# Optimization experiments

Measured on AMD Instinct MI355X. Metric: run time of the kernel, lower is better.

Reference implementation:

```python
import jax, jax.numpy as jnp
import numpy as np

HIDDEN = 256
HEADS = 8
HEAD_DIM = HIDDEN // HEADS
SCALE = HEAD_DIM ** -0.5


def setup_inputs() -> dict:
    key = jax.random.key(0)
    ks = jax.random.split(key, 12)
    B, N = 2, 2048
    s = lambda fan_in: 1.0 / np.sqrt(fan_in)
    inp = {
        'x': jax.random.normal(ks[0], (B, N, HIDDEN), jnp.float32),
        'coords': jax.random.normal(ks[1], (B, N, 3), jnp.float32),
        'W_qkv': jax.random.normal(ks[2], (HIDDEN, 3 * HIDDEN), jnp.float32) * s(HIDDEN),
        'W_out': jax.random.normal(ks[3], (HIDDEN, HIDDEN), jnp.float32) * s(HIDDEN),
        'b_out': jnp.zeros((HIDDEN,), jnp.float32),
        'pos_w1': jax.random.normal(ks[4], (3, 16), jnp.float32) * s(3),
        'pos_b1': jnp.zeros((16,), jnp.float32),
        'pos_w2': jax.random.normal(ks[5], (16, HEADS), jnp.float32) * s(16),
        'pos_b2': jnp.zeros((HEADS,), jnp.float32),
        'sym_w1': jax.random.normal(ks[6], (3, 16), jnp.float32) * s(3),
        'sym_b1': jnp.zeros((16,), jnp.float32),
        'sym_w2': jax.random.normal(ks[7], (16, HEADS), jnp.float32) * s(16),
        'sym_b2': jnp.zeros((HEADS,), jnp.float32),
    }
    return inp


def _bias_mlp(rel, w1, b1, w2, b2):
    # rel: [B,N,N,3] -> [B,H,N,N]
    h = jax.nn.relu(jnp.einsum('bijc,ck->bijk', rel, w1) + b1)
    out = jnp.einsum('bijk,kh->bijh', h, w2) + b2
    return jnp.transpose(out, (0, 3, 1, 2))


def reference(x, coords, W_qkv, W_out, b_out, pos_w1, pos_b1, pos_w2, pos_b2,
              sym_w1, sym_b1, sym_w2, sym_b2):
    B, N, C = x.shape
    qkv = (x @ W_qkv).reshape(B, N, 3, HEADS, HEAD_DIM)
    qkv = jnp.transpose(qkv, (2, 0, 3, 1, 4))  # [3,B,H,N,D]
    q, k, v = qkv[0], qkv[1], qkv[2]
    dots = jnp.einsum('bhid,bhjd->bhij', q, k) * SCALE
    rel_pos = coords[:, :, None, :] - coords[:, None, :, :]  # [B,N,N,3]
    reflect = jnp.array([-1.0, 1.0, 1.0], dtype=coords.dtype)
    coords_sym = coords * reflect
    sym_rel_pos = coords[:, :, None, :] - coords_sym[:, None, :, :]
    bias_direct = _bias_mlp(rel_pos, pos_w1, pos_b1, pos_w2, pos_b2)
    bias_sym = _bias_mlp(sym_rel_pos, sym_w1, sym_b1, sym_w2, sym_b2)
    attn = jax.nn.softmax(dots + bias_direct + bias_sym, axis=-1)
    out = jnp.einsum('bhij,bhjd->bhid', attn, v)
    out = jnp.transpose(out, (0, 2, 1, 3)).reshape(B, N, C)
    return out @ W_out + b_out
```

## Files before the change

kernel.cpp:

```cpp
#include <hip/hip_runtime.h>
#include <hip/hip_fp16.h>

typedef _Float16 half8_t __attribute__((ext_vector_type(8)));
typedef _Float16 half4_t __attribute__((ext_vector_type(4)));
typedef _Float16 h2      __attribute__((ext_vector_type(2)));
typedef float    f32x4   __attribute__((ext_vector_type(4)));

#define LOG2E 1.4426950408889634f
#define KSCALE (0.17677669529663687f * LOG2E)

#if __has_builtin(__builtin_amdgcn_exp2f)
#define EXP2F(x) __builtin_amdgcn_exp2f(x)
#else
#define EXP2F(x) exp2f(x)
#endif

template <int N>
__device__ __forceinline__ int dpp_ror(int v) {
  return __builtin_amdgcn_update_dpp(0, v, 0x120 + N, 0xf, 0xf, true);
}
__device__ __forceinline__ h2 rowmax16_h2(h2 v) {
  int t;
  t = dpp_ror<1>(__builtin_bit_cast(int, v));
  v = __builtin_elementwise_max(v, __builtin_bit_cast(h2, t));
  t = dpp_ror<2>(__builtin_bit_cast(int, v));
  v = __builtin_elementwise_max(v, __builtin_bit_cast(h2, t));
  t = dpp_ror<4>(__builtin_bit_cast(int, v));
  v = __builtin_elementwise_max(v, __builtin_bit_cast(h2, t));
  t = dpp_ror<8>(__builtin_bit_cast(int, v));
  v = __builtin_elementwise_max(v, __builtin_bit_cast(h2, t));
  return v;
}

__global__ __launch_bounds__(256) void prep_misc(
    const float* __restrict__ Wqkv, const float* __restrict__ Wout,
    const float* __restrict__ coords,
    const float* __restrict__ pw1, const float* __restrict__ pb1,
    const float* __restrict__ sw1, const float* __restrict__ sb1,
    _Float16* __restrict__ WqkvT, _Float16* __restrict__ WoutT,
    _Float16* __restrict__ APre, _Float16* __restrict__ BPre)
{
  __shared__ float tile[64][65];
  const int bi = blockIdx.x, tid = threadIdx.x;
  if (bi < 64) {
    const float* src; _Float16* dst; int t, W;
    if (bi < 48) { t = bi;      src = Wqkv; dst = WqkvT; W = 768; }
    else         { t = bi - 48; src = Wout; dst = WoutT; W = 256; }
    const int nOT = W >> 6;
    const int tk = t / nOT, to = t % nOT;
    const int cx = tid & 63, ry = tid >> 6;
#pragma unroll
    for (int rr = 0; rr < 16; ++rr) {
      const int kl = rr * 4 + ry;
      tile[kl][cx] = src[(tk * 64 + kl) * W + to * 64 + cx];
    }
    __syncthreads();
#pragma unroll
    for (int rr = 0; rr < 16; ++rr) {
      const int ol = rr * 4 + ry;
      dst[(to * 64 + ol) * 256 + tk * 64 + cx] = (_Float16)tile[cx][ol];
    }
  } else {
    const int row = (bi - 64) * 256 + tid;
    const float c0 = coords[row * 3 + 0];
    const float c1 = coords[row * 3 + 1];
    const float c2 = coords[row * 3 + 2];
#pragma unroll
    for (int k = 0; k < 16; ++k) {
      float a = c0 * pw1[k] + c1 * pw1[16 + k] + c2 * pw1[32 + k];
      APre[row * 32 + k] = (_Float16)(a + pb1[k]);
      BPre[row * 32 + k] = (_Float16)a;
      float s  =  c0 * sw1[k] + c1 * sw1[16 + k] + c2 * sw1[32 + k];
      float sb = -c0 * sw1[k] + c1 * sw1[16 + k] + c2 * sw1[32 + k];
      APre[row * 32 + 16 + k] = (_Float16)(s + sb1[k]);
      BPre[row * 32 + 16 + k] = (_Float16)sb;
    }
  }
}

__global__ __launch_bounds__(256) void qkv_gemm(
    const float* __restrict__ x, const _Float16* __restrict__ WqkvT,
    _Float16* __restrict__ Qh, _Float16* __restrict__ Kh,
    _Float16* __restrict__ Vt)
{
  __shared__ __align__(16) _Float16 tbuf[4][1536];
  const int wv = threadIdx.x >> 6;
  const int wg = blockIdx.x * 4 + wv;
  const int ti = wg / 12, og = wg % 12;
  const int i0 = ti * 16, o0 = og * 64;
  const int lane = threadIdx.x & 63, q = lane >> 4, c = lane & 15;
  f32x4 acc[4] = {{0,0,0,0},{0,0,0,0},{0,0,0,0},{0,0,0,0}};
  const float*    arow = x + (i0 + c) * 256;
  const _Float16* brow = WqkvT + (o0 + c) * 256;
#pragma unroll
  for (int k0 = 0; k0 < 256; k0 += 32) {
    f32x4 a0 = *reinterpret_cast<const f32x4*>(arow + k0 + q * 8);
    f32x4 a1 = *reinterpret_cast<const f32x4*>(arow + k0 + q * 8 + 4);
    half8_t af;
    af[0] = (_Float16)a0[0]; af[1] = (_Float16)a0[1];
    af[2] = (_Float16)a0[2]; af[3] = (_Float16)a0[3];
    af[4] = (_Float16)a1[0]; af[5] = (_Float16)a1[1];
    af[6] = (_Float16)a1[2]; af[7] = (_Float16)a1[3];
#pragma unroll
    for (int t = 0; t < 4; ++t) {
      half8_t bf = *reinterpret_cast<const half8_t*>(brow + t * 16 * 256 + k0 + q * 8);
      acc[t] = __builtin_amdgcn_mfma_f32_16x16x32_f16(af, bf, acc[t], 0, 0, 0);
    }
  }
  const int b = i0 >> 11, n0 = i0 & 2047;
  _Float16* vt = tbuf[wv];
  if (og < 8) {
#pragma unroll
    for (int t = 0; t < 4; ++t)
#pragma unroll
      for (int r = 0; r < 4; ++r)
        vt[(q * 4 + r) * 72 + t * 16 + c] = (_Float16)acc[t][r];
    asm volatile("s_waitcnt lgkmcnt(0)" ::: "memory");
    __builtin_amdgcn_sched_barrier(0);
    const int nl = lane & 15, seg = lane >> 4;
    const int o_g = o0 + seg * 16;
    const int h = (o_g >> 5) & 7, dbase = o_g & 31;
    _Float16* dst = ((o_g >> 8) == 0 ? Qh : Kh) +
                    ((b * 8 + h) * 2048 + n0 + nl) * 32 + dbase;
    half8_t r0 = *reinterpret_cast<const half8_t*>(vt + nl * 72 + seg * 16);
    half8_t r1 = *reinterpret_cast<const half8_t*>(vt + nl * 72 + seg * 16 + 8);
    *reinterpret_cast<half8_t*>(dst)     = r0;
    *reinterpret_cast<half8_t*>(dst + 8) = r1;
  } else {
#pragma unroll
    for (int t = 0; t < 4; ++t)
#pragma unroll
      for (int r = 0; r < 4; ++r)
        vt[(t * 16 + c) * 24 + q * 4 + r] = (_Float16)acc[t][r];
    asm volatile("s_waitcnt lgkmcnt(0)" ::: "memory");
    __builtin_amdgcn_sched_barrier(0);
    const long row = (long)(b * 256 + (o0 - 512) + lane);
    half8_t r0 = *reinterpret_cast<const half8_t*>(vt + lane * 24);
    half8_t r1 = *reinterpret_cast<const half8_t*>(vt + lane * 24 + 8);
    *reinterpret_cast<half8_t*>(Vt + row * 2048 + n0)     = r0;
    *reinterpret_cast<half8_t*>(Vt + row * 2048 + n0 + 8) = r1;
  }
}

__global__ __launch_bounds__(512, 4) void flash(
    const _Float16* __restrict__ Qh, const _Float16* __restrict__ Kh,
    const _Float16* __restrict__ Vt, const _Float16* __restrict__ APre,
    const _Float16* __restrict__ BPre, const float* __restrict__ pw2,
    const float* __restrict__ sw2, _Float16* __restrict__ Opart,
    float* __restrict__ Mpart)
{
  __shared__ __align__(16) unsigned char smem[53504];
  _Float16* biasH = reinterpret_cast<_Float16*>(smem);
  _Float16* pbuf  = reinterpret_cast<_Float16*>(smem + 37120);

  const int blk = blockIdx.x;
  const int b     = blk >> 8;
  const int chunk = (blk >> 6) & 3;
  const int i0    = (blk & 63) << 5;
  const int tid = threadIdx.x;
  const int w = tid >> 6, lane = tid & 63;
  const int q = lane >> 4, c = lane & 15;

  const _Float16* qbase = Qh + ((b * 8 + w) * 2048 + i0) * 32;
  half8_t qfA = *reinterpret_cast<const half8_t*>(qbase + c * 32 + q * 8);
  half8_t qfB = *reinterpret_cast<const half8_t*>(qbase + (16 + c) * 32 + q * 8);
  const _Float16* abase = APre + (b * 2048 + i0) * 32;
  half8_t apfA = *reinterpret_cast<const half8_t*>(abase + c * 32 + q * 8);
  half8_t apfB = *reinterpret_cast<const half8_t*>(abase + (16 + c) * 32 + q * 8);

  half8_t w2f;
#pragma unroll
  for (int jj = 0; jj < 8; ++jj) {
    const int k = q * 8 + jj;
    float val = 0.f;
    if (c < 8) val = (k < 16 ? pw2[k * 8 + c] : sw2[(k - 16) * 8 + c]) * LOG2E;
    w2f[jj] = (_Float16)val;
  }
  half8_t ones8;
#pragma unroll
  for (int jj = 0; jj < 8; ++jj) ones8[jj] = (_Float16)1.0f;

  float mA[4], mB[4];
  f32x4 O0A = {0,0,0,0}, O1A = {0,0,0,0}, O0B = {0,0,0,0}, O1B = {0,0,0,0};
  f32x4 lpA = {0,0,0,0}, lpB = {0,0,0,0};
#pragma unroll
  for (int r = 0; r < 4; ++r) { mA[r] = 0.f; mB[r] = 0.f; }

  const f32x4 z4 = {0.f, 0.f, 0.f, 0.f};
  half8_t hzero8 = {};

  const int jbase = chunk * 512;
  const _Float16* BPre_b = BPre + (long)b * 2048 * 32;

  const int bwoff = c * 1160 + w * 144 + q * 4;
  const int broff = w * 1160 + c * 72 + q * 4;
  _Float16* pbA = pbuf + w * 1024;
  _Float16* pbB = pbA + 512;
  const int pwo = q * 128 + 2 * c;
  const int pro = c * 32 + q * 8;
  const _Float16* kb0 = Kh + ((b * 8 + w) * 2048 + jbase) * 32;
  const _Float16* vb0 = Vt + (b * 8 + w) * 65536 + jbase;
  const int ko0 = (2 * c) * 32 + q * 8, ko1 = ko0 + 32;
  const int vo0 = c * 2048 + q * 8,     vo1 = vo0 + 16 * 2048;
  const _Float16* bpb = BPre_b + (jbase + w * 4) * 32 + q * 8;

  auto bias_prod = [&](_Float16* bH, half8_t f0, half8_t f1, half8_t f2,
                       half8_t f3) {
    _Float16* bW = bH + bwoff;
#pragma unroll
    for (int mt = 0; mt < 4; ++mt) {
      half8_t bpf = (mt == 0) ? f0 : (mt == 1) ? f1 : (mt == 2) ? f2 : f3;
      half8_t hvA = __builtin_elementwise_max(apfA - bpf, hzero8);
      f32x4 bcA = __builtin_amdgcn_mfma_f32_16x16x32_f16(hvA, w2f, z4, 0, 0, 0);
      half8_t hvB = __builtin_elementwise_max(apfB - bpf, hzero8);
      f32x4 bcB = __builtin_amdgcn_mfma_f32_16x16x32_f16(hvB, w2f, z4, 0, 0, 0);
      if (c < 8) {
        half4_t b4;
        b4[0] = (_Float16)bcA[0]; b4[1] = (_Float16)bcA[1];
        b4[2] = (_Float16)bcA[2]; b4[3] = (_Float16)bcA[3];
        *reinterpret_cast<half4_t*>(bW + mt * 36) = b4;
        half4_t b5;
        b5[0] = (_Float16)bcB[0]; b5[1] = (_Float16)bcB[1];
        b5[2] = (_Float16)bcB[2]; b5[3] = (_Float16)bcB[3];
        *reinterpret_cast<half4_t*>(bW + mt * 36 + 16) = b5;
      }
    }
  };

  {
    half8_t t0 = *reinterpret_cast<const half8_t*>(bpb);
    half8_t t1 = *reinterpret_cast<const half8_t*>(bpb + 32);
    half8_t t2 = *reinterpret_cast<const half8_t*>(bpb + 64);
    half8_t t3 = *reinterpret_cast<const half8_t*>(bpb + 96);
    bias_prod(biasH, t0, t1, t2, t3);
  }
  half8_t pf0 = *reinterpret_cast<const half8_t*>(bpb + 1024);
  half8_t pf1 = *reinterpret_cast<const half8_t*>(bpb + 1024 + 32);
  half8_t pf2 = *reinterpret_cast<const half8_t*>(bpb + 1024 + 64);
  half8_t pf3 = *reinterpret_cast<const half8_t*>(bpb + 1024 + 96);
  __syncthreads();

  auto tile = [&](const int jt, _Float16* bufR, _Float16* bufW,
                  const bool last) {
    const _Float16* bR = bufR + broff;
    half4_t bbA0 = *reinterpret_cast<const half4_t*>(bR);
    half4_t bbA1 = *reinterpret_cast<const half4_t*>(bR + 36);
    half4_t bbB0 = *reinterpret_cast<const half4_t*>(bR + 16);
    half4_t bbB1 = *reinterpret_cast<const half4_t*>(bR + 52);

    if (!last) bias_prod(bufW, pf0, pf1, pf2, pf3);

    {
      const int jn = (jt + 2 < 16) ? (jt + 2) : 15;
      const _Float16* bp = bpb + jn * 1024;
      pf0 = *reinterpret_cast<const half8_t*>(bp);
      pf1 = *reinterpret_cast<const half8_t*>(bp + 32);
      pf2 = *reinterpret_cast<const half8_t*>(bp + 64);
      pf3 = *reinterpret_cast<const half8_t*>(bp + 96);
    }

    const _Float16* kbase = kb0 + jt * 1024;
    const _Float16* vbase = vb0 + jt * 32;
    half8_t kf0 = *reinterpret_cast<const half8_t*>(kbase + ko0);
    half8_t kf1 = *reinterpret_cast<const half8_t*>(kbase + ko1);
    half8_t vf0 = *reinterpret_cast<const half8_t*>(vbase + vo0);
    half8_t vf1 = *reinterpret_cast<const half8_t*>(vbase + vo1);
    f32x4 sA0 = __builtin_amdgcn_mfma_f32_16x16x32_f16(qfA, kf0, z4, 0, 0, 0);
    f32x4 sA1 = __builtin_amdgcn_mfma_f32_16x16x32_f16(qfA, kf1, z4, 0, 0, 0);
    f32x4 sB0 = __builtin_amdgcn_mfma_f32_16x16x32_f16(qfB, kf0, z4, 0, 0, 0);
    f32x4 sB1 = __builtin_amdgcn_mfma_f32_16x16x32_f16(qfB, kf1, z4, 0, 0, 0);

    {
      float svm0[4], svm1[4], p0[4], p1[4];
#pragma unroll
      for (int r = 0; r < 4; ++r) {
        const float bm0 = (float)bbA0[r] - mA[r];
        const float bm1 = (float)bbA1[r] - mA[r];
        svm0[r] = fmaf(sA0[r], KSCALE, bm0);
        svm1[r] = fmaf(sA1[r], KSCALE, bm1);
        p0[r] = EXP2F(svm0[r]);
        p1[r] = EXP2F(svm1[r]);
      }
      float need = fmaxf(fmaxf(fmaxf(svm0[0], svm1[0]), fmaxf(svm0[1], svm1[1])),
                         fmaxf(fmaxf(svm0[2], svm1[2]), fmaxf(svm0[3], svm1[3])));
      if (__any(need > 4.0f)) {
        float mr[4];
#pragma unroll
        for (int r = 0; r < 4; ++r) mr[r] = fmaxf(svm0[r], svm1[r]) + mA[r];
        h2 pk01, pk23;
        pk01[0] = (_Float16)mr[0]; pk01[1] = (_Float16)mr[1];
        pk23[0] = (_Float16)mr[2]; pk23[1] = (_Float16)mr[3];
        pk01 = rowmax16_h2(pk01);
        pk23 = rowmax16_h2(pk23);
        float mred[4] = {(float)pk01[0], (float)pk01[1],
                         (float)pk23[0], (float)pk23[1]};
#pragma unroll
        for (int r = 0; r < 4; ++r) {
          const float mnew = fmaxf(mA[r], mred[r]);
          const float alpha = EXP2F(mA[r] - mnew);
          p0[r] *= alpha; p1[r] *= alpha;
          lpA[r] *= alpha;
          O0A[r] *= alpha; O1A[r] *= alpha;
          mA[r] = mnew;
        }
      }
#pragma unroll
      for (int r = 0; r < 4; ++r) {
        h2 pp; pp[0] = (_Float16)p0[r]; pp[1] = (_Float16)p1[r];
        *reinterpret_cast<h2*>(pbA + pwo + r * 32) = pp;
      }
    }
    {
      float svm0[4], svm1[4], p0[4], p1[4];
#pragma unroll
      for (int r = 0; r < 4; ++r) {
        const float bm0 = (float)bbB0[r] - mB[r];
        const float bm1 = (float)bbB1[r] - mB[r];
        svm0[r] = fmaf(sB0[r], KSCALE, bm0);
        svm1[r] = fmaf(sB1[r], KSCALE, bm1);
        p0[r] = EXP2F(svm0[r]);
        p1[r] = EXP2F(svm1[r]);
      }
      float need = fmaxf(fmaxf(fmaxf(svm0[0], svm1[0]), fmaxf(svm0[1], svm1[1])),
                         fmaxf(fmaxf(svm0[2], svm1[2]), fmaxf(svm0[3], svm1[3])));
      if (__any(need > 4.0f)) {
        float mr[4];
#pragma unroll
        for (int r = 0; r < 4; ++r) mr[r] = fmaxf(svm0[r], svm1[r]) + mB[r];
        h2 pk01, pk23;
        pk01[0] = (_Float16)mr[0]; pk01[1] = (_Float16)mr[1];
        pk23[0] = (_Float16)mr[2]; pk23[1] = (_Float16)mr[3];
        pk01 = rowmax16_h2(pk01);
        pk23 = rowmax16_h2(pk23);
        float mred[4] = {(float)pk01[0], (float)pk01[1],
                         (float)pk23[0], (float)pk23[1]};
#pragma unroll
        for (int r = 0; r < 4; ++r) {
          const float mnew = fmaxf(mB[r], mred[r]);
          const float alpha = EXP2F(mB[r] - mnew);
          p0[r] *= alpha; p1[r] *= alpha;
          lpB[r] *= alpha;
          O0B[r] *= alpha; O1B[r] *= alpha;
          mB[r] = mnew;
        }
      }
#pragma unroll
      for (int r = 0; r < 4; ++r) {
        h2 pp; pp[0] = (_Float16)p0[r]; pp[1] = (_Float16)p1[r];
        *reinterpret_cast<h2*>(pbB + pwo + r * 32) = pp;
      }
    }

    asm volatile("s_waitcnt lgkmcnt(0)" ::: "memory");
    __builtin_amdgcn_sched_barrier(0);

    half8_t pfAx = *reinterpret_cast<const half8_t*>(pbA + pro);
    half8_t pfBx = *reinterpret_cast<const half8_t*>(pbB + pro);
    O0A = __builtin_amdgcn_mfma_f32_16x16x32_f16(pfAx, vf0, O0A, 0, 0, 0);
    O1A = __builtin_amdgcn_mfma_f32_16x16x32_f16(pfAx, vf1, O1A, 0, 0, 0);
    O0B = __builtin_amdgcn_mfma_f32_16x16x32_f16(pfBx, vf0, O0B, 0, 0, 0);
    O1B = __builtin_amdgcn_mfma_f32_16x16x32_f16(pfBx, vf1, O1B, 0, 0, 0);
    lpA = __builtin_amdgcn_mfma_f32_16x16x32_f16(pfAx, ones8, lpA, 0, 0, 0);
    lpB = __builtin_amdgcn_mfma_f32_16x16x32_f16(pfBx, ones8, lpB, 0, 0, 0);

    if (!last) __syncthreads();
  };

  for (int pt = 0; pt < 8; ++pt) {
    tile(2 * pt,     biasH,        biasH + 9280, false);
    tile(2 * pt + 1, biasH + 9280, biasH,        pt == 7);
  }

#pragma unroll
  for (int r = 0; r < 4; ++r) {
    const float s = lpA[r];
    const float inv = 1.f / s;
    const int n = i0 + q * 4 + r;
    const long base = (long)(((chunk * 2 + b) * 8 + w) * 2048 + n);
    Opart[base * 32 + c]      = (_Float16)(O0A[r] * inv);
    Opart[base * 32 + 16 + c] = (_Float16)(O1A[r] * inv);
    if (c == 0) Mpart[base] = mA[r] + __log2f(s);
  }
#pragma unroll
  for (int r = 0; r < 4; ++r) {
    const float s = lpB[r];
    const float inv = 1.f / s;
    const int n = i0 + 16 + q * 4 + r;
    const long base = (long)(((chunk * 2 + b) * 8 + w) * 2048 + n);
    Opart[base * 32 + c]      = (_Float16)(O0B[r] * inv);
    Opart[base * 32 + 16 + c] = (_Float16)(O1B[r] * inv);
    if (c == 0) Mpart[base] = mB[r] + __log2f(s);
  }
}

__global__ __launch_bounds__(256) void combine_proj(
    const _Float16* __restrict__ Opart, const float* __restrict__ Mpart,
    const _Float16* __restrict__ WoutT, const float* __restrict__ bout,
    float* __restrict__ out)
{
  __shared__ _Float16 aT[16][264];
  const int i0 = blockIdx.x * 16;
  const int b = i0 >> 11;
  const int n0 = i0 & 2047;
  const int tid = threadIdx.x;
  {
    const int row = tid >> 4, cg = tid & 15;
    const int n = n0 + row;
    const int h = cg >> 1;
    const int d0 = (cg & 1) * 16;
    float mv[4], M = -INFINITY;
#pragma unroll
    for (int ck = 0; ck < 4; ++ck) {
      mv[ck] = Mpart[((ck * 2 + b) * 8 + h) * 2048 + n];
      M = fmaxf(M, mv[ck]);
    }
    float num[16];
#pragma unroll
    for (int e = 0; e < 16; ++e) num[e] = 0.f;
    float den = 0.f;
#pragma unroll
    for (int ck = 0; ck < 4; ++ck) {
      const float wgt = EXP2F(mv[ck] - M);
      const _Float16* op = Opart +
          (long)(((ck * 2 + b) * 8 + h) * 2048 + n) * 32 + d0;
      half8_t o0v = *reinterpret_cast<const half8_t*>(op);
      half8_t o1v = *reinterpret_cast<const half8_t*>(op + 8);
#pragma unroll
      for (int e = 0; e < 8; ++e) {
        num[e]     += wgt * (float)o0v[e];
        num[8 + e] += wgt * (float)o1v[e];
      }
      den += wgt;
    }
    const float inv = 1.f / den;
    half8_t h0, h1;
#pragma unroll
    for (int e = 0; e < 8; ++e) {
      h0[e] = (_Float16)(num[e] * inv);
      h1[e] = (_Float16)(num[8 + e] * inv);
    }
    *reinterpret_cast<half8_t*>(&aT[row][cg * 16])     = h0;
    *reinterpret_cast<half8_t*>(&aT[row][cg * 16 + 8]) = h1;
  }
  __syncthreads();

  const int o0 = (tid >> 6) * 64;
  const int lane = tid & 63, q = lane >> 4, c = lane & 15;
  f32x4 acc[4] = {{0,0,0,0},{0,0,0,0},{0,0,0,0},{0,0,0,0}};
  const _Float16* brow = WoutT + (o0 + c) * 256;
#pragma unroll
  for (int k0 = 0; k0 < 256; k0 += 32) {
    half8_t af = *reinterpret_cast<const half8_t*>(&aT[c][k0 + q * 8]);
#pragma unroll
    for (int t = 0; t < 4; ++t) {
      half8_t bf = *reinterpret_cast<const half8_t*>(brow + t * 16 * 256 + k0 + q * 8);
      acc[t] = __builtin_amdgcn_mfma_f32_16x16x32_f16(af, bf, acc[t], 0, 0, 0);
    }
  }
#pragma unroll
  for (int t = 0; t < 4; ++t) {
    const float bo = bout[o0 + t * 16 + c];
#pragma unroll
    for (int r = 0; r < 4; ++r)
      out[(i0 + q * 4 + r) * 256 + o0 + t * 16 + c] = acc[t][r] + bo;
  }
}

extern "C" void kernel_launch(void* const* d_in, const int* in_sizes, int n_in,
                              void* d_out, int out_size, void* d_ws, size_t ws_size,
                              hipStream_t stream)
{
  const float* x      = (const float*)d_in[0];
  const float* coords = (const float*)d_in[1];
  const float* Wqkv   = (const float*)d_in[2];
  const float* Wout   = (const float*)d_in[3];
  const float* bout   = (const float*)d_in[4];
  const float* pw1    = (const float*)d_in[5];
  const float* pb1    = (const float*)d_in[6];
  const float* pw2    = (const float*)d_in[7];
  const float* sw1    = (const float*)d_in[9];
  const float* sb1    = (const float*)d_in[10];
  const float* sw2    = (const float*)d_in[11];
  float* out = (float*)d_out;

  char* ws = (char*)d_ws;
  _Float16* Qh      = (_Float16*)(ws + 0);
  _Float16* Kh      = (_Float16*)(ws + 2097152);
  _Float16* Vt      = (_Float16*)(ws + 4194304);
  _Float16* WqkvT   = (_Float16*)(ws + 8388608);
  _Float16* WoutT   = (_Float16*)(ws + 8781824);
  _Float16* APre    = (_Float16*)(ws + 8912896);
  _Float16* BPre    = (_Float16*)(ws + 9175040);
  _Float16* Opart   = (_Float16*)(ws + 9437184);
  float*    Mpart   = (float*)   (ws + 17825792);

  prep_misc<<<80, 256, 0, stream>>>(Wqkv, Wout, coords, pw1, pb1, sw1, sb1,
                                    WqkvT, WoutT, APre, BPre);
  qkv_gemm<<<768, 256, 0, stream>>>(x, WqkvT, Qh, Kh, Vt);
  flash<<<512, 512, 0, stream>>>(Qh, Kh, Vt, APre, BPre, pw2, sw2, Opart, Mpart);
  combine_proj<<<256, 256, 0, stream>>>(Opart, Mpart, WoutT, bout, out);
}
```

Before: 163.6 us.

## Prefetch next K/V fragments and defer bias production until after PV MFMAs

Loads the K and V fragments for the next tile one iteration ahead, so the QK MFMAs no longer wait on global loads. The two A/B softmax halves are merged into one pass that shares a single wave-wide rescale check. The bias MLP production for the tile after next, plus its prefetch, moves after the PV MFMAs so it can overlap with them. This raises register pressure, and reordering the bias writes before the barrier could shift LDS contention.

Result: slower. 202.9 us (+24.0%).

```diff
diff --git a/kernel.cpp b/kernel.cpp
--- a/kernel.cpp
+++ b/kernel.cpp
@@ -227,6 +227,13 @@
     }
   };
 
+  half8_t kfP0, kfP1, vfP0, vfP1;
+  half8_t pf0, pf1, pf2, pf3;
+
+  kfP0 = *reinterpret_cast<const half8_t*>(kb0 + ko0);
+  kfP1 = *reinterpret_cast<const half8_t*>(kb0 + ko1);
+  vfP0 = *reinterpret_cast<const half8_t*>(vb0 + vo0);
+  vfP1 = *reinterpret_cast<const half8_t*>(vb0 + vo1);
   {
     half8_t t0 = *reinterpret_cast<const half8_t*>(bpb);
     half8_t t1 = *reinterpret_cast<const half8_t*>(bpb + 32);
@@ -234,10 +241,10 @@
     half8_t t3 = *reinterpret_cast<const half8_t*>(bpb + 96);
     bias_prod(biasH, t0, t1, t2, t3);
   }
-  half8_t pf0 = *reinterpret_cast<const half8_t*>(bpb + 1024);
-  half8_t pf1 = *reinterpret_cast<const half8_t*>(bpb + 1024 + 32);
-  half8_t pf2 = *reinterpret_cast<const half8_t*>(bpb + 1024 + 64);
-  half8_t pf3 = *reinterpret_cast<const half8_t*>(bpb + 1024 + 96);
+  pf0 = *reinterpret_cast<const half8_t*>(bpb + 1024);
+  pf1 = *reinterpret_cast<const half8_t*>(bpb + 1024 + 32);
+  pf2 = *reinterpret_cast<const half8_t*>(bpb + 1024 + 64);
+  pf3 = *reinterpret_cast<const half8_t*>(bpb + 1024 + 96);
   __syncthreads();
 
   auto tile = [&](const int jt, _Float16* bufR, _Float16* bufW,
@@ -248,107 +255,77 @@
     half4_t bbB0 = *reinterpret_cast<const half4_t*>(bR + 16);
     half4_t bbB1 = *reinterpret_cast<const half4_t*>(bR + 52);
 
-    if (!last) bias_prod(bufW, pf0, pf1, pf2, pf3);
-
-    {
-      const int jn = (jt + 2 < 16) ? (jt + 2) : 15;
-      const _Float16* bp = bpb + jn * 1024;
-      pf0 = *reinterpret_cast<const half8_t*>(bp);
-      pf1 = *reinterpret_cast<const half8_t*>(bp + 32);
-      pf2 = *reinterpret_cast<const half8_t*>(bp + 64);
-      pf3 = *reinterpret_cast<const half8_t*>(bp + 96);
-    }
-
-    const _Float16* kbase = kb0 + jt * 1024;
-    const _Float16* vbase = vb0 + jt * 32;
-    half8_t kf0 = *reinterpret_cast<const half8_t*>(kbase + ko0);
-    half8_t kf1 = *reinterpret_cast<const half8_t*>(kbase + ko1);
-    half8_t vf0 = *reinterpret_cast<const half8_t*>(vbase + vo0);
-    half8_t vf1 = *reinterpret_cast<const half8_t*>(vbase + vo1);
+    half8_t kf0 = kfP0, kf1 = kfP1, vf0 = vfP0, vf1 = vfP1;
     f32x4 sA0 = __builtin_amdgcn_mfma_f32_16x16x32_f16(qfA, kf0, z4, 0, 0, 0);
     f32x4 sA1 = __builtin_amdgcn_mfma_f32_16x16x32_f16(qfA, kf1, z4, 0, 0, 0);
     f32x4 sB0 = __builtin_amdgcn_mfma_f32_16x16x32_f16(qfB, kf0, z4, 0, 0, 0);
     f32x4 sB1 = __builtin_amdgcn_mfma_f32_16x16x32_f16(qfB, kf1, z4, 0, 0, 0);
 
     {
-      float svm0[4], svm1[4], p0[4], p1[4];
-#pragma unroll
-      for (int r = 0; r < 4; ++r) {
-        const float bm0 = (float)bbA0[r] - mA[r];
-        const float bm1 = (float)bbA1[r] - mA[r];
-        svm0[r] = fmaf(sA0[r], KSCALE, bm0);
-        svm1[r] = fmaf(sA1[r], KSCALE, bm1);
-        p0[r] = EXP2F(svm0[r]);
-        p1[r] = EXP2F(svm1[r]);
-      }
-      float need = fmaxf(fmaxf(fmaxf(svm0[0], svm1[0]), fmaxf(svm0[1], svm1[1])),
-                         fmaxf(fmaxf(svm0[2], svm1[2]), fmaxf(svm0[3], svm1[3])));
-      if (__any(need > 4.0f)) {
-        float mr[4];
-#pragma unroll
-        for (int r = 0; r < 4; ++r) mr[r] = fmaxf(svm0[r], svm1[r]) + mA[r];
-        h2 pk01, pk23;
-        pk01[0] = (_Float16)mr[0]; pk01[1] = (_Float16)mr[1];
-        pk23[0] = (_Float16)mr[2]; pk23[1] = (_Float16)mr[3];
-        pk01 = rowmax16_h2(pk01);
-        pk23 = rowmax16_h2(pk23);
-        float mred[4] = {(float)pk01[0], (float)pk01[1],
-                         (float)pk23[0], (float)pk23[1]};
+      const int jn = last ? jt : jt + 1;
+      const _Float16* kbase = kb0 + jn * 1024;
+      const _Float16* vbase = vb0 + jn * 32;
+      kfP0 = *reinterpret_cast<const half8_t*>(kbase + ko0);
+      kfP1 = *reinterpret_cast<const half8_t*>(kbase + ko1);
+      vfP0 = *reinterpret_cast<const half8_t*>(vbase + vo0);
+      vfP1 = *reinterpret_cast<const half8_t*>(vbase + vo1);
+    }
+
+    float pA0[4], pA1[4], pB0[4], pB1[4];
+    float svA0[4], svA1[4], svB0[4], svB1[4];
+#pragma unroll
+    for (int r = 0; r < 4; ++r) {
+      svA0[r] = fmaf(sA0[r], KSCALE, (float)bbA0[r] - mA[r]);
+      svA1[r] = fmaf(sA1[r], KSCALE, (float)bbA1[r] - mA[r]);
+      svB0[r] = fmaf(sB0[r], KSCALE, (float)bbB0[r] - mB[r]);
+      svB1[r] = fmaf(sB1[r], KSCALE, (float)bbB1[r] - mB[r]);
+      pA0[r] = EXP2F(svA0[r]);
+      pA1[r] = EXP2F(svA1[r]);
+      pB0[r] = EXP2F(svB0[r]);
+      pB1[r] = EXP2F(svB1[r]);
+    }
+    {
+      float needA = fmaxf(fmaxf(fmaxf(svA0[0], svA1[0]), fmaxf(svA0[1], svA1[1])),
+                          fmaxf(fmaxf(svA0[2], svA1[2]), fmaxf(svA0[3], svA1[3])));
+      float needB = fmaxf(fmaxf(fmaxf(svB0[0], svB1[0]), fmaxf(svB0[1], svB1[1])),
+                          fmaxf(fmaxf(svB0[2], svB1[2]), fmaxf(svB0[3], svB1[3])));
+      if (__any(fmaxf(needA, needB) > 4.0f)) {
+        float mrA[4], mrB[4];
 #pragma unroll
         for (int r = 0; r < 4; ++r) {
-          const float mnew = fmaxf(mA[r], mred[r]);
-          const float alpha = EXP2F(mA[r] - mnew);
-          p0[r] *= alpha; p1[r] *= alpha;
-          lpA[r] *= alpha;
-          O0A[r] *= alpha; O1A[r] *= alpha;
-          mA[r] = mnew;
+          mrA[r] = fmaxf(svA0[r], svA1[r]) + mA[r];
+          mrB[r] = fmaxf(svB0[r], svB1[r]) + mB[r];
+        }
+        h2 a01, a23, b01, b23;
+        a01[0] = (_Float16)mrA[0]; a01[1] = (_Float16)mrA[1];
+        a23[0] = (_Float16)mrA[2]; a23[1] = (_Float16)mrA[3];
+        b01[0] = (_Float16)mrB[0]; b01[1] = (_Float16)mrB[1];
+        b23[0] = (_Float16)mrB[2]; b23[1] = (_Float16)mrB[3];
+        a01 = rowmax16_h2(a01); a23 = rowmax16_h2(a23);
+        b01 = rowmax16_h2(b01); b23 = rowmax16_h2(b23);
+        float mredA[4] = {(float)a01[0], (float)a01[1], (float)a23[0], (float)a23[1]};
+        float mredB[4] = {(float)b01[0], (float)b01[1], (float)b23[0], (float)b23[1]};
+#pragma unroll
+        for (int r = 0; r < 4; ++r) {
+          const float mnA = fmaxf(mA[r], mredA[r]);
+          const float aA = EXP2F(mA[r] - mnA);
+          pA0[r] *= aA; pA1[r] *= aA;
+          lpA[r] *= aA; O0A[r] *= aA; O1A[r] *= aA;
+          mA[r] = mnA;
+          const float mnB = fmaxf(mB[r], mredB[r]);
+          const float aB = EXP2F(mB[r] - mnB);
+          pB0[r] *= aB; pB1[r] *= aB;
+          lpB[r] *= aB; O0B[r] *= aB; O1B[r] *= aB;
+          mB[r] = mnB;
         }
       }
-#pragma unroll
-      for (int r = 0; r < 4; ++r) {
-        h2 pp; pp[0] = (_Float16)p0[r]; pp[1] = (_Float16)p1[r];
-        *reinterpret_cast<h2*>(pbA + pwo + r * 32) = pp;
-      }
-    }
-    {
-      float svm0[4], svm1[4], p0[4], p1[4];
-#pragma unroll
-      for (int r = 0; r < 4; ++r) {
-        const float bm0 = (float)bbB0[r] - mB[r];
-        const float bm1 = (float)bbB1[r] - mB[r];
-        svm0[r] = fmaf(sB0[r], KSCALE, bm0);
-        svm1[r] = fmaf(sB1[r], KSCALE, bm1);
-        p0[r] = EXP2F(svm0[r]);
-        p1[r] = EXP2F(svm1[r]);
-      }
-      float need = fmaxf(fmaxf(fmaxf(svm0[0], svm1[0]), fmaxf(svm0[1], svm1[1])),
-                         fmaxf(fmaxf(svm0[2], svm1[2]), fmaxf(svm0[3], svm1[3])));
-      if (__any(need > 4.0f)) {
-        float mr[4];
-#pragma unroll
-        for (int r = 0; r < 4; ++r) mr[r] = fmaxf(svm0[r], svm1[r]) + mB[r];
-        h2 pk01, pk23;
-        pk01[0] = (_Float16)mr[0]; pk01[1] = (_Float16)mr[1];
-        pk23[0] = (_Float16)mr[2]; pk23[1] = (_Float16)mr[3];
-        pk01 = rowmax16_h2(pk01);
-        pk23 = rowmax16_h2(pk23);
-        float mred[4] = {(float)pk01[0], (float)pk01[1],
-                         (float)pk23[0], (float)pk23[1]};
-#pragma unroll
-        for (int r = 0; r < 4; ++r) {
-          const float mnew = fmaxf(mB[r], mred[r]);
-          const float alpha = EXP2F(mB[r] - mnew);
-          p0[r] *= alpha; p1[r] *= alpha;
-          lpB[r] *= alpha;
-          O0B[r] *= alpha; O1B[r] *= alpha;
-          mB[r] = mnew;
-        }
-      }
-#pragma unroll
-      for (int r = 0; r < 4; ++r) {
-        h2 pp; pp[0] = (_Float16)p0[r]; pp[1] = (_Float16)p1[r];
-        *reinterpret_cast<h2*>(pbB + pwo + r * 32) = pp;
-      }
+    }
+#pragma unroll
+    for (int r = 0; r < 4; ++r) {
+      h2 ppA; ppA[0] = (_Float16)pA0[r]; ppA[1] = (_Float16)pA1[r];
+      *reinterpret_cast<h2*>(pbA + pwo + r * 32) = ppA;
+      h2 ppB; ppB[0] = (_Float16)pB0[r]; ppB[1] = (_Float16)pB1[r];
+      *reinterpret_cast<h2*>(pbB + pwo + r * 32) = ppB;
     }
 
     asm volatile("s_waitcnt lgkmcnt(0)" ::: "memory");
@@ -363,7 +340,16 @@
     lpA = __builtin_amdgcn_mfma_f32_16x16x32_f16(pfAx, ones8, lpA, 0, 0, 0);
     lpB = __builtin_amdgcn_mfma_f32_16x16x32_f16(pfBx, ones8, lpB, 0, 0, 0);
 
-    if (!last) __syncthreads();
+    if (!last) {
+      bias_prod(bufW, pf0, pf1, pf2, pf3);
+      const int jn = (jt + 2 < 16) ? (jt + 2) : 15;
+      const _Float16* bp = bpb + jn * 1024;
+      pf0 = *reinterpret_cast<const half8_t*>(bp);
+      pf1 = *reinterpret_cast<const half8_t*>(bp + 32);
+      pf2 = *reinterpret_cast<const half8_t*>(bp + 64);
+      pf3 = *reinterpret_cast<const half8_t*>(bp + 96);
+      __syncthreads();
+    }
   };
 
   for (int pt = 0; pt < 8; ++pt) {
```
